# Optimization experiments

Hardware: AMD Instinct MI355X
Metric: run time of the kernel (lower is better)

The kernel has to match this reference:

```python
import jax, jax.numpy as jnp
import numpy as np

N_HEADS = 8
CLIP = 10.0  # tanh_clipping


def setup_inputs() -> dict:
    key = jax.random.key(0)
    ks = jax.random.split(key, 10)
    B, N, d = 2048, 128, 128
    s = 1.0 / np.sqrt(d).astype(np.float32)
    return {
        "h": jax.random.normal(ks[0], (B, N, d), jnp.float32),
        "graph": jax.random.normal(ks[1], (B, d), jnp.float32),
        "Wq": jax.random.normal(ks[2], (d, d), jnp.float32) * s,
        "bq": jax.random.normal(ks[3], (d,), jnp.float32) * s,
        "Wk": jax.random.normal(ks[4], (d, d), jnp.float32) * s,
        "bk": jax.random.normal(ks[5], (d,), jnp.float32) * s,
        "Wv": jax.random.normal(ks[6], (d, d), jnp.float32) * s,
        "bv": jax.random.normal(ks[7], (d,), jnp.float32) * s,
        "Wc": jax.random.normal(ks[8], (2 * d, d), jnp.float32) * s,
        "bc": jax.random.normal(ks[9], (d,), jnp.float32) * s,
    }


def reference(h, graph, Wq, bq, Wk, bk, Wv, bv, Wc, bc):
    # Kool-style pointer decoder, decode_type='sample', start node fixed at 0
    # (equivalent to random_start=False). Sampling keys are fixed JAX PRNG keys.
    B, N, d = h.shape
    H = N_HEADS
    dk = d // H
    sqrt_dk = jnp.sqrt(jnp.float32(dk))

    K = (h @ Wk + bk).reshape(B, N, H, dk)   # [B,N,H,dk]
    V = (h @ Wv + bv).reshape(B, N, H, dk)   # computed but unused, as in original

    bidx = jnp.arange(B)
    cur0 = jnp.zeros((B,), jnp.int32)
    visited0 = jnp.zeros((B, N), bool).at[bidx, cur0].set(True)
    keys = jax.random.split(jax.random.key(42), N - 1)

    def step(carry, key):
        cur, visited, logp_sum = carry
        h_cur = h[bidx, cur]                                  # [B,d] gather of current node
        c = jnp.concatenate([graph, h_cur], axis=-1) @ Wc + bc  # [B,d]
        q = (c @ Wq + bq).reshape(B, H, dk)
        scores = (jnp.einsum('bhk,bnhk->bhn', q, K) / sqrt_dk).mean(axis=1)  # [B,N]
        scores = CLIP * jnp.tanh(scores)
        scores = jnp.where(visited, -jnp.inf, scores)
        nxt = jax.random.categorical(key, scores, axis=-1).astype(jnp.int32)
        logp = jnp.take_along_axis(jax.nn.log_softmax(scores, axis=-1), nxt[:, None], axis=1)[:, 0]
        visited = visited.at[bidx, nxt].set(True)
        return (nxt, visited, logp_sum + logp), nxt

    (_, _, logp_sum), steps = jax.lax.scan(
        step, (cur0, visited0, jnp.zeros((B,), jnp.float32)), keys)
    tour = jnp.concatenate([cur0[:, None], steps.T], axis=1)  # [B,N]
    return tour, logp_sum
```

## Files before the change

### kernel.cpp

```cpp
#include <hip/hip_runtime.h>
#include <cstdint>

#define BB 2048
#define NN 128
#define DD 128
#define CHUNK 1024
#define SW 36

__device__ __forceinline__ void tf_round(uint32_t& x0, uint32_t& x1, int r) {
  x0 += x1; x1 = (x1 << r) | (x1 >> (32 - r)); x1 ^= x0;
}

__device__ __forceinline__ uint2 threefry(uint32_t k0, uint32_t k1, uint32_t x0, uint32_t x1) {
  uint32_t k2 = k0 ^ k1 ^ 0x1BD11BDAu;
  x0 += k0; x1 += k1;
  tf_round(x0,x1,13); tf_round(x0,x1,15); tf_round(x0,x1,26); tf_round(x0,x1,6);
  x0 += k1; x1 += k2 + 1u;
  tf_round(x0,x1,17); tf_round(x0,x1,29); tf_round(x0,x1,16); tf_round(x0,x1,24);
  x0 += k2; x1 += k0 + 2u;
  tf_round(x0,x1,13); tf_round(x0,x1,15); tf_round(x0,x1,26); tf_round(x0,x1,6);
  x0 += k0; x1 += k1 + 3u;
  tf_round(x0,x1,17); tf_round(x0,x1,29); tf_round(x0,x1,16); tf_round(x0,x1,24);
  x0 += k1; x1 += k2 + 4u;
  tf_round(x0,x1,13); tf_round(x0,x1,15); tf_round(x0,x1,26); tf_round(x0,x1,6);
  x0 += k2; x1 += k0 + 5u;
  uint2 r; r.x = x0; r.y = x1; return r;
}

__device__ __forceinline__ float gumbel_from_bits(uint32_t bits) {
  const float TINY = 1.17549435e-38f;
  float u = __uint_as_float(0x3F800000u | (bits >> 9)) - 1.0f;
  u = u + TINY;
  u = fmaxf(TINY, u);
  return -logf(-logf(u));
}

__global__ void k_keys(uint2* __restrict__ keys) {
  int i = threadIdx.x;
  if (i < NN) keys[i] = threefry(0u, 42u, 0u, (uint32_t)i);
}

__global__ void k_M(const float* __restrict__ Wc, const float* __restrict__ Wq,
                    float* __restrict__ M) {
  __shared__ __align__(16) float wrow[DD];
  int r = blockIdx.x, o = threadIdx.x;
  wrow[o] = Wc[(DD + r) * DD + o];
  __syncthreads();
  float acc = 0.f;
#pragma unroll 4
  for (int c = 0; c < DD; ++c) acc += wrow[c] * Wq[c * DD + o];
  M[r * DD + o] = acc;
}

__global__ void k_qbase(const float* __restrict__ graph, const float* __restrict__ Wc,
                        const float* __restrict__ bc, const float* __restrict__ Wq,
                        const float* __restrict__ bq, float* __restrict__ Qbase) {
  __shared__ __align__(16) float g[DD];
  __shared__ __align__(16) float c1[DD];
  int b = blockIdx.x, t = threadIdx.x;
  g[t] = graph[b * DD + t];
  __syncthreads();
  float acc = 0.f;
#pragma unroll 4
  for (int r = 0; r < DD; ++r) acc += g[r] * Wc[r * DD + t];
  c1[t] = acc + bc[t];
  __syncthreads();
  float acc2 = 0.f;
#pragma unroll 4
  for (int c = 0; c < DD; ++c) acc2 += c1[c] * Wq[c * DD + t];
  Qbase[b * DD + t] = acc2 + bq[t];
}

__global__ __launch_bounds__(512, 2) void k_kqq(
    const float* __restrict__ h, const float* __restrict__ Wk, const float* __restrict__ bk,
    const float* __restrict__ Mm, const float* __restrict__ Qbase,
    float* __restrict__ Kc, float* __restrict__ QQc, int b0) {
  __shared__ __align__(16) float As[64 * 32];
  __shared__ __align__(16) float Wks[32 * DD];
  __shared__ __align__(16) float Mms[32 * DD];
  int tid = threadIdx.x;
  int grow0 = b0 * NN + blockIdx.x * 64;
  int ty = tid >> 5, tx = tid & 31;
  float accK[4][4] = {{0}}, accQ[4][4] = {{0}};
  for (int kp = 0; kp < DD; kp += 32) {
    __syncthreads();
    {
      int r = tid >> 3, c4 = (tid & 7) * 4;
      int pc = c4 ^ ((r & 7) * 4);
      *(float4*)&As[r * 32 + pc] = *(const float4*)&h[(size_t)(grow0 + r) * DD + kp + c4];
    }
#pragma unroll
    for (int p = 0; p < 2; ++p) {
      int t = tid + p * 512;
      int r = t >> 5, c4 = (t & 31) * 4;
      *(float4*)&Wks[r * DD + c4] = *(const float4*)&Wk[(size_t)(kp + r) * DD + c4];
      *(float4*)&Mms[r * DD + c4] = *(const float4*)&Mm[(size_t)(kp + r) * DD + c4];
    }
    __syncthreads();
#pragma unroll
    for (int k4 = 0; k4 < 32; k4 += 4) {
      float4 a4[4];
#pragma unroll
      for (int i = 0; i < 4; ++i) {
        int row = ty * 4 + i;
        a4[i] = *(const float4*)&As[row * 32 + (k4 ^ ((row & 7) * 4))];
      }
#pragma unroll
      for (int kk = 0; kk < 4; ++kk) {
        float4 w = *(const float4*)&Wks[(k4 + kk) * DD + tx * 4];
        float4 m = *(const float4*)&Mms[(k4 + kk) * DD + tx * 4];
#pragma unroll
        for (int i = 0; i < 4; ++i) {
          float a = ((const float*)&a4[i])[kk];
          accK[i][0] += a * w.x; accK[i][1] += a * w.y; accK[i][2] += a * w.z; accK[i][3] += a * w.w;
          accQ[i][0] += a * m.x; accQ[i][1] += a * m.y; accQ[i][2] += a * m.z; accQ[i][3] += a * m.w;
        }
      }
    }
  }
  float4 bk4 = *(const float4*)&bk[tx * 4];
#pragma unroll
  for (int i = 0; i < 4; ++i) {
    int grow = grow0 + ty * 4 + i;
    int b = grow >> 7;
    int lrow = grow - b0 * NN;
    float4 qb = *(const float4*)&Qbase[b * DD + tx * 4];
    float4 ok, oq;
    ok.x = accK[i][0] + bk4.x; ok.y = accK[i][1] + bk4.y;
    ok.z = accK[i][2] + bk4.z; ok.w = accK[i][3] + bk4.w;
    oq.x = accQ[i][0] + qb.x;  oq.y = accQ[i][1] + qb.y;
    oq.z = accQ[i][2] + qb.z;  oq.w = accQ[i][3] + qb.w;
    *(float4*)&Kc[lrow * DD + tx * 4] = ok;
    *(float4*)&QQc[lrow * DD + tx * 4] = oq;
  }
}

__global__ __launch_bounds__(512, 2) void k_score(
    const float* __restrict__ QQc, const float* __restrict__ Kc,
    float* __restrict__ T, int b0) {
  __shared__ __align__(16) float QQs[NN * SW];
  __shared__ __align__(16) float Ks[NN * SW];
  int bb = blockIdx.x;
  int tid = threadIdx.x;
  int ty = tid >> 4, tx = tid & 15;
  const float* QQb = QQc + (size_t)bb * NN * DD;
  const float* Kb  = Kc  + (size_t)bb * NN * DD;
  float acc[4][8] = {{0}};
  for (int kp = 0; kp < DD; kp += 32) {
#pragma unroll
    for (int p = 0; p < 2; ++p) {
      int idx = tid + p * 512;
      int row = idx >> 3, c4 = (idx & 7) * 4;
      int pc = c4 ^ (((row >> 3) & 7) * 4);
      *(float4*)&QQs[row * SW + pc] = *(const float4*)&QQb[row * DD + kp + c4];
      *(float4*)&Ks [row * SW + pc] = *(const float4*)&Kb [row * DD + kp + c4];
    }
    __syncthreads();
#pragma unroll 2
    for (int k4 = 0; k4 < 32; k4 += 4) {
      int ca = k4 ^ (((ty >> 1) & 7) * 4);
      int cb = k4 ^ ((tx & 7) * 4);
      float4 a[4];
#pragma unroll
      for (int i = 0; i < 4; ++i) a[i] = *(const float4*)&QQs[(ty * 4 + i) * SW + ca];
      {
        float4 bv[4];
#pragma unroll
        for (int j = 0; j < 4; ++j) bv[j] = *(const float4*)&Ks[(tx * 8 + j) * SW + cb];
#pragma unroll
        for (int i = 0; i < 4; ++i)
#pragma unroll
          for (int j = 0; j < 4; ++j)
            acc[i][j] += a[i].x * bv[j].x + a[i].y * bv[j].y +
                         a[i].z * bv[j].z + a[i].w * bv[j].w;
      }
      {
        float4 bv[4];
#pragma unroll
        for (int j = 0; j < 4; ++j) bv[j] = *(const float4*)&Ks[(tx * 8 + 4 + j) * SW + cb];
#pragma unroll
        for (int i = 0; i < 4; ++i)
#pragma unroll
          for (int j = 0; j < 4; ++j)
            acc[i][4 + j] += a[i].x * bv[j].x + a[i].y * bv[j].y +
                             a[i].z * bv[j].z + a[i].w * bv[j].w;
      }
    }
    __syncthreads();
  }
  int b = b0 + bb;
#pragma unroll
  for (int i = 0; i < 4; ++i) {
    int row = ty * 4 + i;
    float4 o0, o1;
    o0.x = 10.0f * tanhf(acc[i][0] * 0.03125f);
    o0.y = 10.0f * tanhf(acc[i][1] * 0.03125f);
    o0.z = 10.0f * tanhf(acc[i][2] * 0.03125f);
    o0.w = 10.0f * tanhf(acc[i][3] * 0.03125f);
    o1.x = 10.0f * tanhf(acc[i][4] * 0.03125f);
    o1.y = 10.0f * tanhf(acc[i][5] * 0.03125f);
    o1.z = 10.0f * tanhf(acc[i][6] * 0.03125f);
    o1.w = 10.0f * tanhf(acc[i][7] * 0.03125f);
    float* dst = &T[((size_t)b * NN + row) * NN + tx * 8];
    *(float4*)dst = o0;
    *(float4*)(dst + 4) = o1;
  }
}

__global__ __launch_bounds__(256) void k_gumbel(const uint2* __restrict__ keys,
                                                float* __restrict__ G) {
  int idx = blockIdx.x * 256 + threadIdx.x;
  int s = idx >> 18;
  uint32_t cnt = (uint32_t)(idx & ((1 << 18) - 1));
  uint2 k = keys[s];
  uint2 r = threefry(k.x, k.y, 0u, cnt);
  G[idx] = gumbel_from_bits(r.x ^ r.y);
}

__global__ __launch_bounds__(64) void k_decode(
    const float* __restrict__ T, const float* __restrict__ G,
    float* __restrict__ out) {
  int b = blockIdx.x;
  int lane = threadIdx.x;
  bool vis0 = (lane == 0), vis1 = false;
  int cur = 0;
  float lp = 0.f;
  if (lane == 0) out[b * NN] = 0.0f;
  const float* Tb = T + (size_t)b * NN * NN;
  const float* Gb = G + (size_t)b * NN;
  float g0 = Gb[lane];
  float g1 = Gb[lane + 64];
  float sc0 = Tb[lane];
  float sc1 = Tb[lane + 64];
  for (int s = 0; s < NN - 1; ++s) {
    bool u0 = !vis0, u1 = !vis1;
    float v0 = vis0 ? -INFINITY : sc0 + g0;
    float v1 = vis1 ? -INFINITY : sc1 + g1;
    float bvv; int bi;
    if (v1 > v0) { bvv = v1; bi = lane + 64; } else { bvv = v0; bi = lane; }
#pragma unroll
    for (int off = 32; off > 0; off >>= 1) {
      float ov = __shfl_xor(bvv, off);
      int oi = __shfl_xor(bi, off);
      if (ov > bvv || (ov == bvv && oi < bi)) { bvv = ov; bi = oi; }
    }
    int nxt = bi;
    int sn = (s + 1 < NN - 1) ? s + 1 : s;
    float nsc0 = Tb[nxt * NN + lane];
    float nsc1 = Tb[nxt * NN + lane + 64];
    float ng0 = Gb[((size_t)sn << 18) + lane];
    float ng1 = Gb[((size_t)sn << 18) + lane + 64];
    {
      int sel = (nxt >> 6) & 1;
      float xx = sel ? sc1 : sc0;
      float scn = __shfl(xx, nxt & 63);
      float m = fmaxf(u0 ? sc0 : -INFINITY, u1 ? sc1 : -INFINITY);
#pragma unroll
      for (int off = 32; off > 0; off >>= 1) m = fmaxf(m, __shfl_xor(m, off));
      float e = (u0 ? expf(sc0 - m) : 0.f) + (u1 ? expf(sc1 - m) : 0.f);
#pragma unroll
      for (int off = 32; off > 0; off >>= 1) e += __shfl_xor(e, off);
      lp += scn - m - logf(e);
    }
    cur = nxt;
    vis0 = vis0 || (lane == nxt);
    vis1 = vis1 || (lane + 64 == nxt);
    if (lane == 0) out[b * NN + s + 1] = (float)cur;
    sc0 = nsc0; sc1 = nsc1; g0 = ng0; g1 = ng1;
  }
  if (lane == 0) out[BB * NN + b] = lp;
}

extern "C" void kernel_launch(void* const* d_in, const int* in_sizes, int n_in,
                              void* d_out, int out_size, void* d_ws, size_t ws_size,
                              hipStream_t stream) {
  const float* h     = (const float*)d_in[0];
  const float* graph = (const float*)d_in[1];
  const float* Wq    = (const float*)d_in[2];
  const float* bq    = (const float*)d_in[3];
  const float* Wk    = (const float*)d_in[4];
  const float* bk    = (const float*)d_in[5];
  const float* Wc    = (const float*)d_in[8];
  const float* bc    = (const float*)d_in[9];
  float* out = (float*)d_out;

  char* ws = (char*)d_ws;
  uint2* keys  = (uint2*)ws;
  float* Mm    = (float*)(ws + 1024);
  float* Qbase = (float*)(ws + 66560);
  float* T     = (float*)(ws + (size_t)(4 << 20));
  size_t xoff  = (size_t)(4 << 20) + (size_t)BB * NN * NN * 4;
  float* Kc    = (float*)(ws + xoff);
  float* QQc   = (float*)(ws + xoff + (size_t)CHUNK * NN * DD * 4);
  float* G     = (float*)(ws + xoff);

  k_keys<<<1, 128, 0, stream>>>(keys);
  k_M<<<128, 128, 0, stream>>>(Wc, Wq, Mm);
  k_qbase<<<BB, 128, 0, stream>>>(graph, Wc, bc, Wq, bq, Qbase);
  for (int b0 = 0; b0 < BB; b0 += CHUNK) {
    k_kqq<<<CHUNK * NN / 64, 512, 0, stream>>>(h, Wk, bk, Mm, Qbase, Kc, QQc, b0);
    k_score<<<CHUNK, 512, 0, stream>>>(QQc, Kc, T, b0);
  }
  k_gumbel<<<127 * 1024, 256, 0, stream>>>(keys, G);
  k_decode<<<BB, 64, 0, stream>>>(T, G, out);
}
```

Baseline: 826.4 us.

## Fuse score computation with sequential decode, keeping score matrix in LDS

Merges the score kernel and the decode kernel. Each block now writes its 128x128 tanh-clipped score tile into 64KB of dynamic shared memory and then runs the 127-step sampling loop on one wavefront, instead of writing the full score tensor to global memory and reading rows back in a separate kernel. The Gumbel noise is now generated before the chunk loop into the region freed by T. This removes the large global write and reread of scores, but 448 of 512 threads sit idle during the serial decode. The 64KB LDS footprint may also cut per-CU occupancy.

```diff
diff --git a/kernel.cpp b/kernel.cpp
--- a/kernel.cpp
+++ b/kernel.cpp
@@ -135,11 +135,23 @@
   }
 }
 
-__global__ __launch_bounds__(512, 2) void k_score(
+__global__ __launch_bounds__(256) void k_gumbel(const uint2* __restrict__ keys,
+                                                float* __restrict__ G) {
+  int idx = blockIdx.x * 256 + threadIdx.x;
+  int s = idx >> 18;
+  uint32_t cnt = (uint32_t)(idx & ((1 << 18) - 1));
+  uint2 k = keys[s];
+  uint2 r = threefry(k.x, k.y, 0u, cnt);
+  G[idx] = gumbel_from_bits(r.x ^ r.y);
+}
+
+__global__ __launch_bounds__(512, 2) void k_fused(
     const float* __restrict__ QQc, const float* __restrict__ Kc,
-    float* __restrict__ T, int b0) {
-  __shared__ __align__(16) float QQs[NN * SW];
-  __shared__ __align__(16) float Ks[NN * SW];
+    const float* __restrict__ G, float* __restrict__ out, int b0) {
+  extern __shared__ float lds[];
+  float* QQs = lds;
+  float* Ks  = lds + NN * SW;
+  float* Tl  = lds;
   int bb = blockIdx.x;
   int tid = threadIdx.x;
   int ty = tid >> 4, tx = tid & 15;
@@ -188,7 +200,6 @@
     }
     __syncthreads();
   }
-  int b = b0 + bb;
 #pragma unroll
   for (int i = 0; i < 4; ++i) {
     int row = ty * 4 + i;
@@ -201,37 +212,23 @@
     o1.y = 10.0f * tanhf(acc[i][5] * 0.03125f);
     o1.z = 10.0f * tanhf(acc[i][6] * 0.03125f);
     o1.w = 10.0f * tanhf(acc[i][7] * 0.03125f);
-    float* dst = &T[((size_t)b * NN + row) * NN + tx * 8];
+    float* dst = &Tl[row * NN + tx * 8];
     *(float4*)dst = o0;
     *(float4*)(dst + 4) = o1;
   }
-}
-
-__global__ __launch_bounds__(256) void k_gumbel(const uint2* __restrict__ keys,
-                                                float* __restrict__ G) {
-  int idx = blockIdx.x * 256 + threadIdx.x;
-  int s = idx >> 18;
-  uint32_t cnt = (uint32_t)(idx & ((1 << 18) - 1));
-  uint2 k = keys[s];
-  uint2 r = threefry(k.x, k.y, 0u, cnt);
-  G[idx] = gumbel_from_bits(r.x ^ r.y);
-}
-
-__global__ __launch_bounds__(64) void k_decode(
-    const float* __restrict__ T, const float* __restrict__ G,
-    float* __restrict__ out) {
-  int b = blockIdx.x;
-  int lane = threadIdx.x;
+  __syncthreads();
+  if (tid >= 64) return;
+  int lane = tid;
+  int b = b0 + bb;
   bool vis0 = (lane == 0), vis1 = false;
   int cur = 0;
   float lp = 0.f;
   if (lane == 0) out[b * NN] = 0.0f;
-  const float* Tb = T + (size_t)b * NN * NN;
   const float* Gb = G + (size_t)b * NN;
   float g0 = Gb[lane];
   float g1 = Gb[lane + 64];
-  float sc0 = Tb[lane];
-  float sc1 = Tb[lane + 64];
+  float sc0 = Tl[lane];
+  float sc1 = Tl[lane + 64];
   for (int s = 0; s < NN - 1; ++s) {
     bool u0 = !vis0, u1 = !vis1;
     float v0 = vis0 ? -INFINITY : sc0 + g0;
@@ -246,8 +243,8 @@
     }
     int nxt = bi;
     int sn = (s + 1 < NN - 1) ? s + 1 : s;
-    float nsc0 = Tb[nxt * NN + lane];
-    float nsc1 = Tb[nxt * NN + lane + 64];
+    float nsc0 = Tl[nxt * NN + lane];
+    float nsc1 = Tl[nxt * NN + lane + 64];
     float ng0 = Gb[((size_t)sn << 18) + lane];
     float ng1 = Gb[((size_t)sn << 18) + lane + 64];
     {
@@ -288,19 +285,17 @@
   uint2* keys  = (uint2*)ws;
   float* Mm    = (float*)(ws + 1024);
   float* Qbase = (float*)(ws + 66560);
-  float* T     = (float*)(ws + (size_t)(4 << 20));
+  float* G     = (float*)(ws + (size_t)(4 << 20));
   size_t xoff  = (size_t)(4 << 20) + (size_t)BB * NN * NN * 4;
   float* Kc    = (float*)(ws + xoff);
   float* QQc   = (float*)(ws + xoff + (size_t)CHUNK * NN * DD * 4);
-  float* G     = (float*)(ws + xoff);
 
   k_keys<<<1, 128, 0, stream>>>(keys);
   k_M<<<128, 128, 0, stream>>>(Wc, Wq, Mm);
   k_qbase<<<BB, 128, 0, stream>>>(graph, Wc, bc, Wq, bq, Qbase);
+  k_gumbel<<<127 * 1024, 256, 0, stream>>>(keys, G);
   for (int b0 = 0; b0 < BB; b0 += CHUNK) {
     k_kqq<<<CHUNK * NN / 64, 512, 0, stream>>>(h, Wk, bk, Mm, Qbase, Kc, QQc, b0);
-    k_score<<<CHUNK, 512, 0, stream>>>(QQc, Kc, T, b0);
-  }
-  k_gumbel<<<127 * 1024, 256, 0, stream>>>(keys, G);
-  k_decode<<<BB, 64, 0, stream>>>(T, G, out);
-}
+    k_fused<<<CHUNK, 512, 65536, stream>>>(QQc, Kc, G, out, b0);
+  }
+}
```

Measured after the change: 1.198 ms. 1.45x slower.

## Run gumbel and decode per chunk, ping-ponging T and G buffers

Applied to the files above, without the earlier changes.

Gumbel noise generation and decoding now run inside the per-chunk loop, next to the K/QQ projection and scoring. T and G each take one half of a workspace region, and the halves swap roles between the two chunks. The aim is a smaller live working set per phase so the score and noise data are more likely to stay cache-resident when decode reads them. The cost is that decode becomes two launches of 1024 single-wave blocks run one after the other, which can stretch the serial, latency-bound decode loop.

```diff
diff --git a/kernel.cpp b/kernel.cpp
--- a/kernel.cpp
+++ b/kernel.cpp
@@ -137,7 +137,7 @@
 
 __global__ __launch_bounds__(512, 2) void k_score(
     const float* __restrict__ QQc, const float* __restrict__ Kc,
-    float* __restrict__ T, int b0) {
+    float* __restrict__ T) {
   __shared__ __align__(16) float QQs[NN * SW];
   __shared__ __align__(16) float Ks[NN * SW];
   int bb = blockIdx.x;
@@ -188,7 +188,6 @@
     }
     __syncthreads();
   }
-  int b = b0 + bb;
 #pragma unroll
   for (int i = 0; i < 4; ++i) {
     int row = ty * 4 + i;
@@ -201,17 +200,18 @@
     o1.y = 10.0f * tanhf(acc[i][5] * 0.03125f);
     o1.z = 10.0f * tanhf(acc[i][6] * 0.03125f);
     o1.w = 10.0f * tanhf(acc[i][7] * 0.03125f);
-    float* dst = &T[((size_t)b * NN + row) * NN + tx * 8];
+    float* dst = &T[((size_t)bb * NN + row) * NN + tx * 8];
     *(float4*)dst = o0;
     *(float4*)(dst + 4) = o1;
   }
 }
 
 __global__ __launch_bounds__(256) void k_gumbel(const uint2* __restrict__ keys,
-                                                float* __restrict__ G) {
+                                                float* __restrict__ G, int b0) {
   int idx = blockIdx.x * 256 + threadIdx.x;
-  int s = idx >> 18;
-  uint32_t cnt = (uint32_t)(idx & ((1 << 18) - 1));
+  int s = idx >> 17;
+  int local = idx & ((1 << 17) - 1);
+  uint32_t cnt = (uint32_t)(b0 * NN + local);
   uint2 k = keys[s];
   uint2 r = threefry(k.x, k.y, 0u, cnt);
   G[idx] = gumbel_from_bits(r.x ^ r.y);
@@ -219,15 +219,16 @@
 
 __global__ __launch_bounds__(64) void k_decode(
     const float* __restrict__ T, const float* __restrict__ G,
-    float* __restrict__ out) {
-  int b = blockIdx.x;
+    float* __restrict__ out, int b0) {
+  int bb = blockIdx.x;
+  int b = b0 + bb;
   int lane = threadIdx.x;
   bool vis0 = (lane == 0), vis1 = false;
   int cur = 0;
   float lp = 0.f;
   if (lane == 0) out[b * NN] = 0.0f;
-  const float* Tb = T + (size_t)b * NN * NN;
-  const float* Gb = G + (size_t)b * NN;
+  const float* Tb = T + (size_t)bb * NN * NN;
+  const float* Gb = G + (size_t)bb * NN;
   float g0 = Gb[lane];
   float g1 = Gb[lane + 64];
   float sc0 = Tb[lane];
@@ -248,8 +249,8 @@
     int sn = (s + 1 < NN - 1) ? s + 1 : s;
     float nsc0 = Tb[nxt * NN + lane];
     float nsc1 = Tb[nxt * NN + lane + 64];
-    float ng0 = Gb[((size_t)sn << 18) + lane];
-    float ng1 = Gb[((size_t)sn << 18) + lane + 64];
+    float ng0 = Gb[((size_t)sn << 17) + lane];
+    float ng1 = Gb[((size_t)sn << 17) + lane + 64];
     {
       int sel = (nxt >> 6) & 1;
       float xx = sel ? sc1 : sc0;
@@ -288,19 +289,22 @@
   uint2* keys  = (uint2*)ws;
   float* Mm    = (float*)(ws + 1024);
   float* Qbase = (float*)(ws + 66560);
-  float* T     = (float*)(ws + (size_t)(4 << 20));
+  float* half0 = (float*)(ws + (size_t)(4 << 20));
+  float* half1 = (float*)(ws + (size_t)(4 << 20) + (size_t)CHUNK * NN * NN * 4);
   size_t xoff  = (size_t)(4 << 20) + (size_t)BB * NN * NN * 4;
   float* Kc    = (float*)(ws + xoff);
   float* QQc   = (float*)(ws + xoff + (size_t)CHUNK * NN * DD * 4);
-  float* G     = (float*)(ws + xoff);
 
   k_keys<<<1, 128, 0, stream>>>(keys);
   k_M<<<128, 128, 0, stream>>>(Wc, Wq, Mm);
   k_qbase<<<BB, 128, 0, stream>>>(graph, Wc, bc, Wq, bq, Qbase);
-  for (int b0 = 0; b0 < BB; b0 += CHUNK) {
+  for (int c = 0; c < 2; ++c) {
+    int b0 = c * CHUNK;
+    float* Tc = c ? half1 : half0;
+    float* Gc = c ? half0 : half1;
+    k_gumbel<<<127 * 512, 256, 0, stream>>>(keys, Gc, b0);
     k_kqq<<<CHUNK * NN / 64, 512, 0, stream>>>(h, Wk, bk, Mm, Qbase, Kc, QQc, b0);
-    k_score<<<CHUNK, 512, 0, stream>>>(QQc, Kc, T, b0);
-  }
-  k_gumbel<<<127 * 1024, 256, 0, stream>>>(keys, G);
-  k_decode<<<BB, 64, 0, stream>>>(T, G, out);
-}
+    k_score<<<CHUNK, 512, 0, stream>>>(QQc, Kc, Tc);
+    k_decode<<<CHUNK, 64, 0, stream>>>(Tc, Gc, out, b0);
+  }
+}
```

Result: slower. 929.1 us (+12.4%).
